# Performance work log

Measured on AMD Instinct MI355X. Metric: run time of the kernel, lower is better.

The kernel has to match this reference:

```python
import jax, jax.numpy as jnp
import numpy as np

L, CIN, CKV, E, H, D, NQ, NK = 3, 128, 256, 128, 8, 16, 4096, 1024
CLAMP_MAX = 65503.0  # torch.clamp(max=65503)
SCALE = 1.0 / (D * D)  # non-standard: 1 / projection_dim**2


def group_norm(x, w, b, groups, eps=1e-5):
    # x: [..., C, N]; w, b broadcastable to x.shape[:-1] (i.e. lead + (C,))
    lead = x.shape[:-2]
    C, N = x.shape[-2:]
    xg = x.reshape(lead + (groups, C // groups, N))
    mu = xg.mean(axis=(-2, -1), keepdims=True)
    var = ((xg - mu) ** 2).mean(axis=(-2, -1), keepdims=True)
    xn = ((xg - mu) * jax.lax.rsqrt(var + eps)).reshape(lead + (C, N))
    return xn * w[..., None] + b[..., None]


def split_heads(t):
    # [L, 1, E, N] -> [L, 1, H, N, D]
    l, b, e, n = t.shape
    return t.transpose(0, 1, 3, 2).reshape(l, b, n, H, D).transpose(0, 1, 3, 2, 4)


def setup_inputs():
    key = jax.random.key(0)
    ks = jax.random.split(key, 18)
    r = lambda k, s: jax.random.normal(k, s, dtype=jnp.float32)
    return {
        'x': r(ks[0], (1, CIN, NQ)),
        'x_global': r(ks[1], (L, CKV, NK)),
        'xyz': r(ks[2], (1, NQ, 3)),
        'xyz_global': r(ks[3], (L, NK, 3)),
        'gn1_w': r(ks[4], (CIN,)), 'gn1_b': r(ks[5], (CIN,)),
        'gn2_w': r(ks[6], (L, CKV)), 'gn2_b': r(ks[7], (L, CKV)),
        'qw': r(ks[8], (L, E, CIN)) * 0.05, 'qb': r(ks[9], (L, E)),
        'kw': r(ks[10], (L, E, CKV)) * 0.05, 'kb': r(ks[11], (L, E)),
        'vw': r(ks[12], (L, E, CKV)) * 0.05, 'vb': r(ks[13], (L, E)),
        'qgn_w': r(ks[14], (L, E)), 'qgn_b': r(ks[15], (L, E)),
        'cw': r(ks[16], (L, CIN, E)) * 0.05, 'cb': r(ks[17], (L, CIN)),
    }


def reference(x, x_global, xyz, xyz_global, gn1_w, gn1_b, gn2_w, gn2_b,
              qw, qb, kw, kb, vw, vb, qgn_w, qgn_b, cw, cb):
    # pre-norm of query features (shared across layers): [1, CIN, NQ]
    xq = jax.nn.relu(group_norm(x, gn1_w, gn1_b, 8))
    # per-source KV features: [L, 1, CKV, NK]
    xg = jax.nn.relu(group_norm(x_global[:, None], gn2_w[:, None], gn2_b[:, None], 16))

    # conv1d (kernel=1) projections + the shared q_gn GroupNorm(8, E)
    q = jnp.einsum('lec,bcn->lben', qw, xq) + qb[:, None, :, None]        # [L,1,E,NQ]
    q = group_norm(q, qgn_w[:, None], qgn_b[:, None], 8)
    k = jnp.einsum('lec,lbcn->lben', kw, xg) + kb[:, None, :, None]       # [L,1,E,NK]
    k = group_norm(k, qgn_w[:, None], qgn_b[:, None], 8)
    v = jnp.einsum('lec,lbcn->lben', vw, xg) + vb[:, None, :, None]       # [L,1,E,NK]
    v = group_norm(v, qgn_w[:, None], qgn_b[:, None], 8)

    qh, kh, vh = split_heads(q), split_heads(k), split_heads(v)           # [L,1,H,*,D]

    score = jnp.einsum('lbhqd,lbhkd->lbhqk', qh * SCALE, kh)              # [L,1,H,NQ,NK]
    score = jnp.minimum(score, CLAMP_MAX)
    w_att = jax.nn.softmax(score, axis=-1)
    o = jnp.einsum('lbhqk,lbhkd->lbhqd', w_att, vh)                        # [L,1,H,NQ,D]
    o = o.transpose(0, 1, 3, 2, 4).reshape(L, 1, NQ, E)                    # merge heads
    o = jnp.einsum('lbqe,loe->lbqo', o, cw) + cb[:, None, None, :]         # combine heads
    o = o.transpose(0, 1, 3, 2) + xq[None]                                 # [L,1,CIN,NQ], SA residual

    out = o.mean(axis=0) + x                                               # mean over sources + block residual
    return out, w_att[-1]                                                  # weight of last layer, as in torch loop
```

## Files before the change

kernel.cpp:

```cpp
#include <hip/hip_runtime.h>
#include <math.h>

constexpr int NQ = 4096, NK = 1024, CIN = 128, CKV = 256, E = 128, H = 8, D = 16, LAYERS = 3;
constexpr float SCALE = 1.0f / 256.0f;
constexpr float CLAMP_MAX = 65503.0f;
constexpr float LOG2E = 1.44269504088896340736f;
constexpr float CLAMP2 = CLAMP_MAX * LOG2E;

typedef __bf16 bf16x8 __attribute__((ext_vector_type(8)));
typedef __bf16 bf16x4 __attribute__((ext_vector_type(4)));
typedef float f32x16 __attribute__((ext_vector_type(16)));
typedef float f32x4 __attribute__((ext_vector_type(4)));

__device__ __forceinline__ float exp2_fast(float x) {
#if __has_builtin(__builtin_amdgcn_exp2f)
  return __builtin_amdgcn_exp2f(x);
#else
  return exp2f(x);
#endif
}

__device__ __forceinline__ void block_reduce2(float& a, float& b, float* red) {
#pragma unroll
  for (int off = 32; off > 0; off >>= 1) {
    a += __shfl_down(a, off, 64);
    b += __shfl_down(b, off, 64);
  }
  int lane = threadIdx.x & 63, wid = threadIdx.x >> 6;
  if (lane == 0) { red[wid * 2] = a; red[wid * 2 + 1] = b; }
  __syncthreads();
  if (threadIdx.x == 0) {
    float sa = 0.f, sb = 0.f;
#pragma unroll
    for (int w = 0; w < 4; w++) { sa += red[w * 2]; sb += red[w * 2 + 1]; }
    red[0] = sa; red[1] = sb;
  }
  __syncthreads();
  a = red[0]; b = red[1];
}

__global__ __launch_bounds__(256) void pre_partial(const float* __restrict__ x,
                                                   const float* __restrict__ xg,
                                                   float* __restrict__ acc) {
  __shared__ float red[8];
  int b = blockIdx.x, t = threadIdx.x;
  const float4* p;
  int aidx;
  if (b < 256) { p = (const float4*)x + (size_t)b * 512; aidx = b >> 5; }
  else { int i = b - 256; p = (const float4*)xg + (size_t)i * 512; aidx = 8 + (i >> 3); }
  float s = 0.f, sq = 0.f;
#pragma unroll
  for (int i = 0; i < 2; i++) {
    float4 v = p[t + i * 256];
    s += v.x + v.y + v.z + v.w;
    sq += v.x * v.x + v.y * v.y + v.z * v.z + v.w * v.w;
  }
  block_reduce2(s, sq, red);
  if (t == 0) {
    atomicAdd(&acc[aidx * 2], s);
    atomicAdd(&acc[aidx * 2 + 1], sq);
  }
}

__global__ __launch_bounds__(256) void stage_a(const float* __restrict__ x,
                                               const float* __restrict__ xg,
                                               const float* __restrict__ acc,
                                               const float* __restrict__ gn1w,
                                               const float* __restrict__ gn1b,
                                               const float* __restrict__ gn2w,
                                               const float* __restrict__ gn2b,
                                               const float* __restrict__ qw,
                                               const float* __restrict__ kw,
                                               const float* __restrict__ vw,
                                               __bf16* __restrict__ xq_t,
                                               __bf16* __restrict__ xg_t,
                                               __bf16* __restrict__ qwb,
                                               __bf16* __restrict__ kwb,
                                               __bf16* __restrict__ vwb) {
  int b = blockIdx.x, t = threadIdx.x;
  if (b >= 320) {
    int i = b - 320;
    const float* src; __bf16* dst; int off;
    if (i < 24)      { src = qw; dst = qwb; off = i * 2048; }
    else if (i < 72) { src = kw; dst = kwb; off = (i - 24) * 2048; }
    else             { src = vw; dst = vwb; off = (i - 72) * 2048; }
    int base = off + t * 8;
    float4 a = *(const float4*)(src + base);
    float4 c = *(const float4*)(src + base + 4);
    bf16x8 o = { (__bf16)a.x, (__bf16)a.y, (__bf16)a.z, (__bf16)a.w,
                 (__bf16)c.x, (__bf16)c.y, (__bf16)c.z, (__bf16)c.w };
    *(bf16x8*)(dst + base) = o;
    return;
  }
  __shared__ float T[128 * 36];
  const float* in; __bf16* out; int N, Cout, ccbase, n0, gbase;
  const float* gw; const float* gb; float inv;
  if (b < 128) {
    in = x; N = NQ; out = xq_t; Cout = 128; ccbase = 0; n0 = b * 32;
    gw = gn1w; gb = gn1b; gbase = 0; inv = 1.f / 65536.f;
  } else {
    int i = b - 128; int l = i / 64; int r = i % 64; int ch = r >> 5;
    n0 = (r & 31) * 32;
    in = xg + ((size_t)l * 256 + ch * 128) * 1024; N = NK;
    out = xg_t + (size_t)l * 1024 * 256; Cout = 256; ccbase = ch * 128;
    gw = gn2w + l * 256 + ch * 128; gb = gn2b + l * 256 + ch * 128;
    gbase = 8 + l * 16 + ch * 8; inv = 1.f / 16384.f;
  }
  int nq = t & 7, cbase = t >> 3;
#pragma unroll
  for (int i = 0; i < 4; i++) {
    int c = cbase + 32 * i;
    int g = gbase + (c >> 4);
    float mu = acc[2 * g] * inv;
    float rs = rsqrtf(acc[2 * g + 1] * inv - mu * mu + 1e-5f);
    float sc = gw[c] * rs, sh = gb[c] - mu * sc;
    float4 v = *(const float4*)(in + (size_t)c * N + n0 + nq * 4);
    float4 o;
    o.x = fmaxf(v.x * sc + sh, 0.f);
    o.y = fmaxf(v.y * sc + sh, 0.f);
    o.z = fmaxf(v.z * sc + sh, 0.f);
    o.w = fmaxf(v.w * sc + sh, 0.f);
    *(float4*)(T + c * 36 + nq * 4) = o;
  }
  __syncthreads();
  int n = t >> 3, c0 = (t & 7) * 16;
  bf16x8 o1, o2;
#pragma unroll
  for (int j = 0; j < 8; j++) {
    o1[j] = (__bf16)T[(c0 + j) * 36 + n];
    o2[j] = (__bf16)T[(c0 + 8 + j) * 36 + n];
  }
  __bf16* op = out + (size_t)(n0 + n) * Cout + ccbase + c0;
  *(bf16x8*)op = o1;
  *(bf16x8*)(op + 8) = o2;
}

template <int KSTEPS>
__device__ __forceinline__ void gemm_tile(const __bf16* __restrict__ A,
                                          const __bf16* __restrict__ Bm,
                                          int stride, f32x16& acc, int l31, int half) {
#pragma unroll
  for (int ks = 0; ks < KSTEPS; ks++) {
    bf16x8 af = *(const bf16x8*)(A + (size_t)l31 * stride + ks * 16 + half * 8);
    bf16x8 bf = *(const bf16x8*)(Bm + (size_t)l31 * stride + ks * 16 + half * 8);
    acc = __builtin_amdgcn_mfma_f32_32x32x16_bf16(af, bf, acc, 0, 0, 0);
  }
}

__global__ __launch_bounds__(256) void proj_mfma(const __bf16* __restrict__ xq_t,
                                                 const __bf16* __restrict__ xg_t,
                                                 const __bf16* __restrict__ qwb,
                                                 const __bf16* __restrict__ kwb,
                                                 const __bf16* __restrict__ vwb,
                                                 const float* __restrict__ qb,
                                                 const float* __restrict__ kb,
                                                 const float* __restrict__ vb,
                                                 __bf16* __restrict__ q_raw,
                                                 __bf16* __restrict__ k_raw,
                                                 __bf16* __restrict__ v_raw,
                                                 float* __restrict__ qgnAcc) {
  int t = threadIdx.x;
  int w = blockIdx.x * 4 + (t >> 6);
  int lane = t & 63, l31 = lane & 31, half = lane >> 5;
  f32x16 acc = {0.f,0.f,0.f,0.f,0.f,0.f,0.f,0.f,0.f,0.f,0.f,0.f,0.f,0.f,0.f,0.f};
  int mat, l, e0, n0, N;
  const __bf16* A; const __bf16* Bm; const float* bias;
  if (w < 1536) {
    mat = 0; l = w >> 9; int r = w & 511; e0 = (r & 3) * 32; n0 = (r >> 2) * 32;
    N = NQ; A = qwb + (size_t)l * 128 * 128; Bm = xq_t; bias = qb + l * 128;
  } else if (w < 1920) {
    mat = 1; int idx = w - 1536; l = idx >> 7; int r = idx & 127;
    e0 = (r & 3) * 32; n0 = (r >> 2) * 32;
    N = NK; A = kwb + (size_t)l * 128 * 256; Bm = xg_t + (size_t)l * 1024 * 256;
    bias = kb + l * 128;
  } else {
    mat = 2; int idx = w - 1920; l = idx >> 7; int r = idx & 127;
    e0 = (r & 3) * 32; n0 = (r >> 2) * 32;
    N = NK; A = vwb + (size_t)l * 128 * 256; Bm = xg_t + (size_t)l * 1024 * 256;
    bias = vb + l * 128;
  }
  if (mat == 0) {
    gemm_tile<8>(A + (size_t)e0 * 128, Bm + (size_t)n0 * 128, 128, acc, l31, half);
  } else {
    gemm_tile<16>(A + (size_t)e0 * 256, Bm + (size_t)n0 * 256, 256, acc, l31, half);
  }

  float vals[16];
  float s0 = 0.f, sq0 = 0.f, s1 = 0.f, sq1 = 0.f;
#pragma unroll
  for (int r = 0; r < 16; r++) {
    int row = (r & 3) + 8 * (r >> 2) + 4 * half;
    float v = acc[r] + bias[e0 + row];
    vals[r] = v;
    if (r < 8) { s0 += v; sq0 += v * v; } else { s1 += v; sq1 += v * v; }
  }
#pragma unroll
  for (int off = 1; off < 64; off <<= 1) {
    s0 += __shfl_xor(s0, off); sq0 += __shfl_xor(sq0, off);
    s1 += __shfl_xor(s1, off); sq1 += __shfl_xor(sq1, off);
  }
  int gbase = (mat == 0 ? 0 : (mat == 1 ? 24 : 48)) + l * 8 + (e0 >> 4);
  if (lane == 0) {
    atomicAdd(&qgnAcc[gbase * 2], s0);
    atomicAdd(&qgnAcc[gbase * 2 + 1], sq0);
    atomicAdd(&qgnAcc[(gbase + 1) * 2], s1);
    atomicAdd(&qgnAcc[(gbase + 1) * 2 + 1], sq1);
  }
  if (mat < 2) {
    __bf16* out = (mat == 0 ? q_raw : k_raw);
#pragma unroll
    for (int qd = 0; qd < 4; qd++) {
      int h = (e0 >> 4) + (qd >> 1);
      int d0 = 4 * half + 8 * (qd & 1);
      bf16x4 o;
#pragma unroll
      for (int j = 0; j < 4; j++) o[j] = (__bf16)vals[qd * 4 + j];
      *(bf16x4*)(out + ((size_t)(l * 8 + h) * N + n0 + l31) * 16 + d0) = o;
    }
  } else {
#pragma unroll
    for (int r = 0; r < 16; r++) {
      int row = (r & 3) + 8 * (r >> 2) + 4 * half;
      int h = (e0 >> 4) + (row >> 4);
      v_raw[((size_t)(l * 8 + h) * 16 + (row & 15)) * NK + n0 + l31] = (__bf16)vals[r];
    }
  }
}

__global__ __launch_bounds__(256) void qkv_affine(__bf16* __restrict__ q_raw,
                                                  __bf16* __restrict__ k_raw,
                                                  __bf16* __restrict__ v_raw,
                                                  const float* __restrict__ acc,
                                                  const float* __restrict__ gw,
                                                  const float* __restrict__ gb) {
  int b = blockIdx.x, t = threadIdx.x;
  if (b < 768) {
    int v8 = b * 256 + t;
    int d0 = (v8 & 1) * 8;
    int lh = (v8 >> 1) >> 12;
    int l = lh >> 3, h = lh & 7;
    int g = l * 8 + h;
    const float inv = 1.f / 65536.f;
    float mu = acc[2 * g] * inv;
    float rs = rsqrtf(acc[2 * g + 1] * inv - mu * mu + 1e-5f);
    const float EX = SCALE * LOG2E;
    bf16x8 vv = *(bf16x8*)(q_raw + (size_t)v8 * 8);
    bf16x8 o;
#pragma unroll
    for (int j = 0; j < 8; j++) {
      int cidx = l * 128 + h * 16 + d0 + j;
      float w0 = gw[cidx] * rs;
      o[j] = (__bf16)(((float)vv[j] * w0 + (gb[cidx] - mu * w0)) * EX);
    }
    *(bf16x8*)(q_raw + (size_t)v8 * 8) = o;
  } else if (b < 960) {
    int v8 = (b - 768) * 256 + t;
    int d0 = (v8 & 1) * 8;
    int lh = (v8 >> 1) >> 10;
    int l = lh >> 3, h = lh & 7;
    int g = 24 + l * 8 + h;
    const float inv = 1.f / 16384.f;
    float mu = acc[2 * g] * inv;
    float rs = rsqrtf(acc[2 * g + 1] * inv - mu * mu + 1e-5f);
    bf16x8 vv = *(bf16x8*)(k_raw + (size_t)v8 * 8);
    bf16x8 o;
#pragma unroll
    for (int j = 0; j < 8; j++) {
      int cidx = l * 128 + h * 16 + d0 + j;
      float w0 = gw[cidx] * rs;
      o[j] = (__bf16)((float)vv[j] * w0 + (gb[cidx] - mu * w0));
    }
    *(bf16x8*)(k_raw + (size_t)v8 * 8) = o;
  } else {
    int v8 = (b - 960) * 256 + t;
    int rest = v8 >> 7;
    int d = rest & 15, lh = rest >> 4;
    int l = lh >> 3, h = lh & 7;
    int g = 48 + l * 8 + h;
    const float inv = 1.f / 16384.f;
    float mu = acc[2 * g] * inv;
    float rs = rsqrtf(acc[2 * g + 1] * inv - mu * mu + 1e-5f);
    int cidx = l * 128 + h * 16 + d;
    float w0 = gw[cidx] * rs;
    float sh = gb[cidx] - mu * w0;
    bf16x8 vv = *(bf16x8*)(v_raw + (size_t)v8 * 8);
    bf16x8 o;
#pragma unroll
    for (int j = 0; j < 8; j++) o[j] = (__bf16)((float)vv[j] * w0 + sh);
    *(bf16x8*)(v_raw + (size_t)v8 * 8) = o;
  }
}

__global__ __launch_bounds__(256) void attn_kernel(const __bf16* __restrict__ qbf,
                                                   const __bf16* __restrict__ kbf,
                                                   const __bf16* __restrict__ vbf,
                                                   float* __restrict__ ob,
                                                   float* __restrict__ rinv_ws) {
  __shared__ __bf16 Pt[4][32 * 40];
  __shared__ float rinv_s[4][32];

  const int t = threadIdx.x;
  const int wv = t >> 6;
  const int lane = t & 63;
  const int l31 = lane & 31, half = lane >> 5, l15 = lane & 15, quad = lane >> 4;
  const int h = blockIdx.y, l = blockIdx.z;
  const int q0 = blockIdx.x * 128 + wv * 32;

  const __bf16* Qh = qbf + (size_t)(l * H + h) * NQ * D;
  const __bf16* Kh = kbf + (size_t)(l * H + h) * NK * D;
  const __bf16* Vh = vbf + (size_t)(l * H + h) * D * NK;

  const bf16x8 qfrag = *(const bf16x8*)(Qh + (size_t)(q0 + l31) * D + half * 8);

  f32x4 oa0 = {0.f, 0.f, 0.f, 0.f}, oa1 = {0.f, 0.f, 0.f, 0.f};
  float rsum[16];
#pragma unroll
  for (int r = 0; r < 16; ++r) rsum[r] = 0.f;

  __bf16* Pw = &Pt[wv][0];

  for (int c = 0; c < 32; ++c) {
    const int k0 = c * 32;
    bf16x8 kf = *(const bf16x8*)(Kh + (size_t)(k0 + l31) * D + half * 8);
    f32x16 s = {0.f,0.f,0.f,0.f,0.f,0.f,0.f,0.f,0.f,0.f,0.f,0.f,0.f,0.f,0.f,0.f};
    s = __builtin_amdgcn_mfma_f32_32x32x16_bf16(qfrag, kf, s, 0, 0, 0);
#pragma unroll
    for (int r = 0; r < 16; ++r) {
      float p = exp2_fast(fminf(s[r], CLAMP2));
      rsum[r] += p;
      int row = (r & 3) + 8 * (r >> 2) + 4 * half;
      Pw[row * 40 + l31] = (__bf16)p;
    }
    bf16x8 a0 = *(const bf16x8*)(Pw + l15 * 40 + quad * 8);
    bf16x8 a1 = *(const bf16x8*)(Pw + (16 + l15) * 40 + quad * 8);
    bf16x8 bv = *(const bf16x8*)(Vh + (size_t)l15 * NK + k0 + quad * 8);
    oa0 = __builtin_amdgcn_mfma_f32_16x16x32_bf16(a0, bv, oa0, 0, 0, 0);
    oa1 = __builtin_amdgcn_mfma_f32_16x16x32_bf16(a1, bv, oa1, 0, 0, 0);
  }

#pragma unroll
  for (int r = 0; r < 16; ++r) {
    float v = rsum[r];
    v += __shfl_xor(v, 1); v += __shfl_xor(v, 2); v += __shfl_xor(v, 4);
    v += __shfl_xor(v, 8); v += __shfl_xor(v, 16);
    rsum[r] = v;
  }
  if (l31 == 0) {
#pragma unroll
    for (int r = 0; r < 16; ++r)
      rinv_s[wv][(r & 3) + 8 * (r >> 2) + 4 * half] = 1.f / rsum[r];
  }

  float* Ow = (float*)Pw;
#pragma unroll
  for (int r = 0; r < 4; ++r) {
    int qa = quad * 4 + r;
    Ow[l15 * 36 + qa] = oa0[r] * rinv_s[wv][qa];
    Ow[l15 * 36 + 16 + qa] = oa1[r] * rinv_s[wv][16 + qa];
  }
  if (l == 2 && lane < 32)
    rinv_ws[(size_t)h * NQ + q0 + lane] = rinv_s[wv][lane];
  {
    int dd = lane >> 2, j = (lane & 3) * 8;
    float4 u0 = *(const float4*)(Ow + dd * 36 + j);
    float4 u1 = *(const float4*)(Ow + dd * 36 + j + 4);
    size_t rb = (size_t)(l * E + h * D + dd) * NQ + q0 + j;
    *(float4*)(ob + rb) = u0;
    *(float4*)(ob + rb + 4) = u1;
  }
}

__global__ __launch_bounds__(256) void wout_kernel(const __bf16* __restrict__ qbf,
                                                   const __bf16* __restrict__ kbf,
                                                   const float* __restrict__ rinv_ws,
                                                   float* __restrict__ wout) {
  const int t = threadIdx.x;
  const int wv = t >> 6;
  const int lane = t & 63;
  const int l31 = lane & 31, half = lane >> 5;
  const int h = blockIdx.y;
  const int q0 = blockIdx.x * 128 + wv * 32;
  const int kbase = blockIdx.z * 512;

  const __bf16* Qh = qbf + (size_t)(2 * H + h) * NQ * D;
  const __bf16* Kh = kbf + (size_t)(2 * H + h) * NK * D;
  const bf16x8 qfrag = *(const bf16x8*)(Qh + (size_t)(q0 + l31) * D + half * 8);

  float riv[16];
#pragma unroll
  for (int r = 0; r < 16; ++r)
    riv[r] = rinv_ws[(size_t)h * NQ + q0 + (r & 3) + 8 * (r >> 2) + 4 * half];

  for (int c = 0; c < 16; ++c) {
    const int k0 = kbase + c * 32;
    bf16x8 kf = *(const bf16x8*)(Kh + (size_t)(k0 + l31) * D + half * 8);
    f32x16 s = {0.f,0.f,0.f,0.f,0.f,0.f,0.f,0.f,0.f,0.f,0.f,0.f,0.f,0.f,0.f,0.f};
    s = __builtin_amdgcn_mfma_f32_32x32x16_bf16(qfrag, kf, s, 0, 0, 0);
#pragma unroll
    for (int r = 0; r < 16; ++r) {
      float p = exp2_fast(fminf(s[r], CLAMP2)) * riv[r];
      int row = (r & 3) + 8 * (r >> 2) + 4 * half;
      __builtin_nontemporal_store(p, &wout[(size_t)(h * NQ + q0 + row) * NK + k0 + l31]);
    }
  }
}

__global__ __launch_bounds__(256) void combine_kernel(const float* __restrict__ x,
                                                      const float* __restrict__ acc,
                                                      const float* __restrict__ gn1w,
                                                      const float* __restrict__ gn1b,
                                                      const float* __restrict__ ob,
                                                      const float* __restrict__ cw,
                                                      const float* __restrict__ cb,
                                                      float* __restrict__ out) {
  __shared__ float S[128 * 16];
  const int t = threadIdx.x;
  const int nt0 = blockIdx.x * 16;
  const int c0 = (t >> 2) * 2;
  const int nf = t & 3;
  float4 a0 = make_float4(0.f, 0.f, 0.f, 0.f);
  float4 a1 = make_float4(0.f, 0.f, 0.f, 0.f);
  for (int l = 0; l < LAYERS; l++) {
    if (l) __syncthreads();
#pragma unroll
    for (int i = 0; i < 2; i++) {
      int fid = i * 256 + t;
      int e = fid >> 2, pos = fid & 3;
      *(float4*)(S + e * 16 + pos * 4) =
          *(const float4*)(ob + ((size_t)l * E + e) * NQ + nt0 + pos * 4);
    }
    __syncthreads();
    const float* cwl = cw + (size_t)l * CIN * E;
#pragma unroll 8
    for (int e4 = 0; e4 < E / 4; e4++) {
      const int e = e4 * 4;
      float4 w0 = *(const float4*)(cwl + (size_t)c0 * E + e);
      float4 w1 = *(const float4*)(cwl + (size_t)(c0 + 1) * E + e);
      float4 s0 = *(const float4*)(S + (e + 0) * 16 + nf * 4);
      float4 s1 = *(const float4*)(S + (e + 1) * 16 + nf * 4);
      float4 s2 = *(const float4*)(S + (e + 2) * 16 + nf * 4);
      float4 s3 = *(const float4*)(S + (e + 3) * 16 + nf * 4);
      a0.x += w0.x * s0.x + w0.y * s1.x + w0.z * s2.x + w0.w * s3.x;
      a0.y += w0.x * s0.y + w0.y * s1.y + w0.z * s2.y + w0.w * s3.y;
      a0.z += w0.x * s0.z + w0.y * s1.z + w0.z * s2.z + w0.w * s3.z;
      a0.w += w0.x * s0.w + w0.y * s1.w + w0.z * s2.w + w0.w * s3.w;
      a1.x += w1.x * s0.x + w1.y * s1.x + w1.z * s2.x + w1.w * s3.x;
      a1.y += w1.x * s0.y + w1.y * s1.y + w1.z * s2.y + w1.w * s3.y;
      a1.z += w1.x * s0.z + w1.y * s1.z + w1.z * s2.z + w1.w * s3.z;
      a1.w += w1.x * s0.w + w1.y * s1.w + w1.z * s2.w + w1.w * s3.w;
    }
  }
  const float third = 1.f / 3.f;
#pragma unroll
  for (int i = 0; i < 2; i++) {
    int c = c0 + i;
    float4 a = i ? a1 : a0;
    float bsum = (cb[c] + cb[CIN + c] + cb[2 * CIN + c]) * third;
    int g = c >> 4;
    const float inv = 1.f / 65536.f;
    float mu = acc[2 * g] * inv;
    float rs = rsqrtf(acc[2 * g + 1] * inv - mu * mu + 1e-5f);
    float sc = gn1w[c] * rs, sh = gn1b[c] - mu * sc;
    size_t off = (size_t)c * NQ + nt0 + nf * 4;
    float4 xv = *(const float4*)(x + off);
    float4 o;
    o.x = xv.x + fmaxf(xv.x * sc + sh, 0.f) + a.x * third + bsum;
    o.y = xv.y + fmaxf(xv.y * sc + sh, 0.f) + a.y * third + bsum;
    o.z = xv.z + fmaxf(xv.z * sc + sh, 0.f) + a.z * third + bsum;
    o.w = xv.w + fmaxf(xv.w * sc + sh, 0.f) + a.w * third + bsum;
    *(float4*)(out + off) = o;
  }
}

extern "C" void kernel_launch(void* const* d_in, const int* in_sizes, int n_in,
                              void* d_out, int out_size, void* d_ws, size_t ws_size,
                              hipStream_t stream) {
  (void)in_sizes; (void)n_in; (void)out_size;
  const float* x    = (const float*)d_in[0];
  const float* xgi  = (const float*)d_in[1];
  const float* gn1w = (const float*)d_in[4];
  const float* gn1b = (const float*)d_in[5];
  const float* gn2w = (const float*)d_in[6];
  const float* gn2b = (const float*)d_in[7];
  const float* qw   = (const float*)d_in[8];
  const float* qb   = (const float*)d_in[9];
  const float* kw   = (const float*)d_in[10];
  const float* kb   = (const float*)d_in[11];
  const float* vw   = (const float*)d_in[12];
  const float* vb   = (const float*)d_in[13];
  const float* qgnw = (const float*)d_in[14];
  const float* qgnb = (const float*)d_in[15];
  const float* cw   = (const float*)d_in[16];
  const float* cb   = (const float*)d_in[17];

  float* ws = (float*)d_ws;
  __bf16* xq_t  = (__bf16*)ws;
  __bf16* xg_t  = (__bf16*)(ws + 262144);
  __bf16* qwb   = (__bf16*)(ws + 655360);
  __bf16* kwb   = (__bf16*)(ws + 679936);
  __bf16* vwb   = (__bf16*)(ws + 729088);
  __bf16* q_raw = (__bf16*)(ws + 778240);
  __bf16* k_raw = (__bf16*)(ws + 1564672);
  __bf16* v_raw = (__bf16*)(ws + 1761280);
  float*  ob    = ws + 1957888;
  float*  accAll = ws + 3530752;
  float*  rinv_ws = ws + 3531008;
  if (ws_size < (size_t)3563776 * sizeof(float)) return;

  float* qgnAcc = accAll + 112;
  float* outp = (float*)d_out;
  float* wout = outp + 524288;

  hipMemsetAsync(accAll, 0, 256 * sizeof(float), stream);

  pre_partial<<<640, 256, 0, stream>>>(x, xgi, accAll);

  stage_a<<<440, 256, 0, stream>>>(x, xgi, accAll, gn1w, gn1b, gn2w, gn2b,
                                   qw, kw, vw, xq_t, xg_t, qwb, kwb, vwb);

  proj_mfma<<<576, 256, 0, stream>>>(xq_t, xg_t, qwb, kwb, vwb, qb, kb, vb,
                                     q_raw, k_raw, v_raw, qgnAcc);

  qkv_affine<<<1152, 256, 0, stream>>>(q_raw, k_raw, v_raw, qgnAcc, qgnw, qgnb);

  attn_kernel<<<dim3(32, 8, 3), 256, 0, stream>>>(q_raw, k_raw, v_raw, ob, rinv_ws);

  combine_kernel<<<256, 256, 0, stream>>>(x, accAll, gn1w, gn1b, ob, cw, cb, outp);

  wout_kernel<<<dim3(32, 8, 2), 256, 0, stream>>>(q_raw, k_raw, rinv_ws, wout);
}
```

Measured before the change: 302.3 us.

## Fuse q/k/v group-norm affine into attention and merge combine with wout

Removes the separate qkv_affine pass and applies the q_gn normalization on the fly: Q once per fragment, K and V per chunk inside the attention and wout loops. It also merges combine_kernel and wout_kernel into one launch, split by block index. This removes a read-modify-write pass over q/k/v and two kernel launches. In exchange, K and V are renormalized redundantly by every query block, which adds per-iteration ALU work in the inner loop.

```diff
diff --git a/kernel.cpp b/kernel.cpp
--- a/kernel.cpp
+++ b/kernel.cpp
@@ -227,73 +227,12 @@
   }
 }
 
-__global__ __launch_bounds__(256) void qkv_affine(__bf16* __restrict__ q_raw,
-                                                  __bf16* __restrict__ k_raw,
-                                                  __bf16* __restrict__ v_raw,
-                                                  const float* __restrict__ acc,
-                                                  const float* __restrict__ gw,
-                                                  const float* __restrict__ gb) {
-  int b = blockIdx.x, t = threadIdx.x;
-  if (b < 768) {
-    int v8 = b * 256 + t;
-    int d0 = (v8 & 1) * 8;
-    int lh = (v8 >> 1) >> 12;
-    int l = lh >> 3, h = lh & 7;
-    int g = l * 8 + h;
-    const float inv = 1.f / 65536.f;
-    float mu = acc[2 * g] * inv;
-    float rs = rsqrtf(acc[2 * g + 1] * inv - mu * mu + 1e-5f);
-    const float EX = SCALE * LOG2E;
-    bf16x8 vv = *(bf16x8*)(q_raw + (size_t)v8 * 8);
-    bf16x8 o;
-#pragma unroll
-    for (int j = 0; j < 8; j++) {
-      int cidx = l * 128 + h * 16 + d0 + j;
-      float w0 = gw[cidx] * rs;
-      o[j] = (__bf16)(((float)vv[j] * w0 + (gb[cidx] - mu * w0)) * EX);
-    }
-    *(bf16x8*)(q_raw + (size_t)v8 * 8) = o;
-  } else if (b < 960) {
-    int v8 = (b - 768) * 256 + t;
-    int d0 = (v8 & 1) * 8;
-    int lh = (v8 >> 1) >> 10;
-    int l = lh >> 3, h = lh & 7;
-    int g = 24 + l * 8 + h;
-    const float inv = 1.f / 16384.f;
-    float mu = acc[2 * g] * inv;
-    float rs = rsqrtf(acc[2 * g + 1] * inv - mu * mu + 1e-5f);
-    bf16x8 vv = *(bf16x8*)(k_raw + (size_t)v8 * 8);
-    bf16x8 o;
-#pragma unroll
-    for (int j = 0; j < 8; j++) {
-      int cidx = l * 128 + h * 16 + d0 + j;
-      float w0 = gw[cidx] * rs;
-      o[j] = (__bf16)((float)vv[j] * w0 + (gb[cidx] - mu * w0));
-    }
-    *(bf16x8*)(k_raw + (size_t)v8 * 8) = o;
-  } else {
-    int v8 = (b - 960) * 256 + t;
-    int rest = v8 >> 7;
-    int d = rest & 15, lh = rest >> 4;
-    int l = lh >> 3, h = lh & 7;
-    int g = 48 + l * 8 + h;
-    const float inv = 1.f / 16384.f;
-    float mu = acc[2 * g] * inv;
-    float rs = rsqrtf(acc[2 * g + 1] * inv - mu * mu + 1e-5f);
-    int cidx = l * 128 + h * 16 + d;
-    float w0 = gw[cidx] * rs;
-    float sh = gb[cidx] - mu * w0;
-    bf16x8 vv = *(bf16x8*)(v_raw + (size_t)v8 * 8);
-    bf16x8 o;
-#pragma unroll
-    for (int j = 0; j < 8; j++) o[j] = (__bf16)((float)vv[j] * w0 + sh);
-    *(bf16x8*)(v_raw + (size_t)v8 * 8) = o;
-  }
-}
-
 __global__ __launch_bounds__(256) void attn_kernel(const __bf16* __restrict__ qbf,
                                                    const __bf16* __restrict__ kbf,
                                                    const __bf16* __restrict__ vbf,
+                                                   const float* __restrict__ qgnAcc,
+                                                   const float* __restrict__ qgnw,
+                                                   const float* __restrict__ qgnb,
                                                    float* __restrict__ ob,
                                                    float* __restrict__ rinv_ws) {
   __shared__ __bf16 Pt[4][32 * 40];
@@ -310,7 +249,32 @@
   const __bf16* Kh = kbf + (size_t)(l * H + h) * NK * D;
   const __bf16* Vh = vbf + (size_t)(l * H + h) * D * NK;
 
-  const bf16x8 qfrag = *(const bf16x8*)(Qh + (size_t)(q0 + l31) * D + half * 8);
+  const int gq = l * 8 + h, gk = 24 + l * 8 + h, gv = 48 + l * 8 + h;
+  const float invq = 1.f / 65536.f, invkv = 1.f / 16384.f;
+  const float muq = qgnAcc[2 * gq] * invq;
+  const float rsq = rsqrtf(qgnAcc[2 * gq + 1] * invq - muq * muq + 1e-5f);
+  const float muk = qgnAcc[2 * gk] * invkv;
+  const float rsk = rsqrtf(qgnAcc[2 * gk + 1] * invkv - muk * muk + 1e-5f);
+  const float muv = qgnAcc[2 * gv] * invkv;
+  const float rsv = rsqrtf(qgnAcc[2 * gv + 1] * invkv - muv * muv + 1e-5f);
+
+  const int cbase = l * 128 + h * 16;
+  float ka[8], kc[8];
+  bf16x8 qfrag;
+  {
+    const float EX = SCALE * LOG2E;
+    bf16x8 qraw = *(const bf16x8*)(Qh + (size_t)(q0 + l31) * D + half * 8);
+#pragma unroll
+    for (int j = 0; j < 8; j++) {
+      float w = qgnw[cbase + half * 8 + j], bb = qgnb[cbase + half * 8 + j];
+      float wq = w * rsq;
+      qfrag[j] = (__bf16)((float)qraw[j] * (wq * EX) + (bb - muq * wq) * EX);
+      float wk = w * rsk;
+      ka[j] = wk; kc[j] = bb - muk * wk;
+    }
+  }
+  const float va = qgnw[cbase + l15] * rsv;
+  const float vc = qgnb[cbase + l15] - muv * va;
 
   f32x4 oa0 = {0.f, 0.f, 0.f, 0.f}, oa1 = {0.f, 0.f, 0.f, 0.f};
   float rsum[16];
@@ -321,7 +285,10 @@
 
   for (int c = 0; c < 32; ++c) {
     const int k0 = c * 32;
-    bf16x8 kf = *(const bf16x8*)(Kh + (size_t)(k0 + l31) * D + half * 8);
+    bf16x8 kraw = *(const bf16x8*)(Kh + (size_t)(k0 + l31) * D + half * 8);
+    bf16x8 kf;
+#pragma unroll
+    for (int j = 0; j < 8; j++) kf[j] = (__bf16)((float)kraw[j] * ka[j] + kc[j]);
     f32x16 s = {0.f,0.f,0.f,0.f,0.f,0.f,0.f,0.f,0.f,0.f,0.f,0.f,0.f,0.f,0.f,0.f};
     s = __builtin_amdgcn_mfma_f32_32x32x16_bf16(qfrag, kf, s, 0, 0, 0);
 #pragma unroll
@@ -331,9 +298,12 @@
       int row = (r & 3) + 8 * (r >> 2) + 4 * half;
       Pw[row * 40 + l31] = (__bf16)p;
     }
+    bf16x8 vraw = *(const bf16x8*)(Vh + (size_t)l15 * NK + k0 + quad * 8);
+    bf16x8 bv;
+#pragma unroll
+    for (int j = 0; j < 8; j++) bv[j] = (__bf16)((float)vraw[j] * va + vc);
     bf16x8 a0 = *(const bf16x8*)(Pw + l15 * 40 + quad * 8);
     bf16x8 a1 = *(const bf16x8*)(Pw + (16 + l15) * 40 + quad * 8);
-    bf16x8 bv = *(const bf16x8*)(Vh + (size_t)l15 * NK + k0 + quad * 8);
     oa0 = __builtin_amdgcn_mfma_f32_16x16x32_bf16(a0, bv, oa0, 0, 0, 0);
     oa1 = __builtin_amdgcn_mfma_f32_16x16x32_bf16(a1, bv, oa1, 0, 0, 0);
   }
@@ -370,52 +340,80 @@
   }
 }
 
-__global__ __launch_bounds__(256) void wout_kernel(const __bf16* __restrict__ qbf,
+__global__ __launch_bounds__(256) void post_kernel(const __bf16* __restrict__ qbf,
                                                    const __bf16* __restrict__ kbf,
                                                    const float* __restrict__ rinv_ws,
+                                                   const float* __restrict__ qgnAcc,
+                                                   const float* __restrict__ qgnw,
+                                                   const float* __restrict__ qgnb,
+                                                   const float* __restrict__ x,
+                                                   const float* __restrict__ accAll,
+                                                   const float* __restrict__ gn1w,
+                                                   const float* __restrict__ gn1b,
+                                                   const float* __restrict__ ob,
+                                                   const float* __restrict__ cw,
+                                                   const float* __restrict__ cb,
+                                                   float* __restrict__ out,
                                                    float* __restrict__ wout) {
-  const int t = threadIdx.x;
-  const int wv = t >> 6;
-  const int lane = t & 63;
-  const int l31 = lane & 31, half = lane >> 5;
-  const int h = blockIdx.y;
-  const int q0 = blockIdx.x * 128 + wv * 32;
-  const int kbase = blockIdx.z * 512;
-
-  const __bf16* Qh = qbf + (size_t)(2 * H + h) * NQ * D;
-  const __bf16* Kh = kbf + (size_t)(2 * H + h) * NK * D;
-  const bf16x8 qfrag = *(const bf16x8*)(Qh + (size_t)(q0 + l31) * D + half * 8);
-
-  float riv[16];
-#pragma unroll
-  for (int r = 0; r < 16; ++r)
-    riv[r] = rinv_ws[(size_t)h * NQ + q0 + (r & 3) + 8 * (r >> 2) + 4 * half];
-
-  for (int c = 0; c < 16; ++c) {
-    const int k0 = kbase + c * 32;
-    bf16x8 kf = *(const bf16x8*)(Kh + (size_t)(k0 + l31) * D + half * 8);
-    f32x16 s = {0.f,0.f,0.f,0.f,0.f,0.f,0.f,0.f,0.f,0.f,0.f,0.f,0.f,0.f,0.f,0.f};
-    s = __builtin_amdgcn_mfma_f32_32x32x16_bf16(qfrag, kf, s, 0, 0, 0);
-#pragma unroll
-    for (int r = 0; r < 16; ++r) {
-      float p = exp2_fast(fminf(s[r], CLAMP2)) * riv[r];
-      int row = (r & 3) + 8 * (r >> 2) + 4 * half;
-      __builtin_nontemporal_store(p, &wout[(size_t)(h * NQ + q0 + row) * NK + k0 + l31]);
-    }
-  }
-}
-
-__global__ __launch_bounds__(256) void combine_kernel(const float* __restrict__ x,
-                                                      const float* __restrict__ acc,
-                                                      const float* __restrict__ gn1w,
-                                                      const float* __restrict__ gn1b,
-                                                      const float* __restrict__ ob,
-                                                      const float* __restrict__ cw,
-                                                      const float* __restrict__ cb,
-                                                      float* __restrict__ out) {
   __shared__ float S[128 * 16];
-  const int t = threadIdx.x;
-  const int nt0 = blockIdx.x * 16;
+  const int blk = blockIdx.x, t = threadIdx.x;
+  if (blk < 512) {
+    const int wv = t >> 6, lane = t & 63;
+    const int l31 = lane & 31, half = lane >> 5;
+    const int qtile = blk & 31, h = (blk >> 5) & 7, khalf = blk >> 8;
+    const int q0 = qtile * 128 + wv * 32;
+    const int kbase = khalf * 512;
+
+    const __bf16* Qh = qbf + (size_t)(2 * H + h) * NQ * D;
+    const __bf16* Kh = kbf + (size_t)(2 * H + h) * NK * D;
+
+    const int gq = 16 + h, gk = 24 + 16 + h;
+    const float invq = 1.f / 65536.f, invkv = 1.f / 16384.f;
+    const float muq = qgnAcc[2 * gq] * invq;
+    const float rsq = rsqrtf(qgnAcc[2 * gq + 1] * invq - muq * muq + 1e-5f);
+    const float muk = qgnAcc[2 * gk] * invkv;
+    const float rsk = rsqrtf(qgnAcc[2 * gk + 1] * invkv - muk * muk + 1e-5f);
+
+    const int cbase = 2 * 128 + h * 16;
+    float ka[8], kc[8];
+    bf16x8 qfrag;
+    {
+      const float EX = SCALE * LOG2E;
+      bf16x8 qraw = *(const bf16x8*)(Qh + (size_t)(q0 + l31) * D + half * 8);
+#pragma unroll
+      for (int j = 0; j < 8; j++) {
+        float w = qgnw[cbase + half * 8 + j], bb = qgnb[cbase + half * 8 + j];
+        float wq = w * rsq;
+        qfrag[j] = (__bf16)((float)qraw[j] * (wq * EX) + (bb - muq * wq) * EX);
+        float wk = w * rsk;
+        ka[j] = wk; kc[j] = bb - muk * wk;
+      }
+    }
+
+    float riv[16];
+#pragma unroll
+    for (int r = 0; r < 16; ++r)
+      riv[r] = rinv_ws[(size_t)h * NQ + q0 + (r & 3) + 8 * (r >> 2) + 4 * half];
+
+    for (int c = 0; c < 16; ++c) {
+      const int k0 = kbase + c * 32;
+      bf16x8 kraw = *(const bf16x8*)(Kh + (size_t)(k0 + l31) * D + half * 8);
+      bf16x8 kf;
+#pragma unroll
+      for (int j = 0; j < 8; j++) kf[j] = (__bf16)((float)kraw[j] * ka[j] + kc[j]);
+      f32x16 s = {0.f,0.f,0.f,0.f,0.f,0.f,0.f,0.f,0.f,0.f,0.f,0.f,0.f,0.f,0.f,0.f};
+      s = __builtin_amdgcn_mfma_f32_32x32x16_bf16(qfrag, kf, s, 0, 0, 0);
+#pragma unroll
+      for (int r = 0; r < 16; ++r) {
+        float p = exp2_fast(fminf(s[r], CLAMP2)) * riv[r];
+        int row = (r & 3) + 8 * (r >> 2) + 4 * half;
+        __builtin_nontemporal_store(p, &wout[(size_t)(h * NQ + q0 + row) * NK + k0 + l31]);
+      }
+    }
+    return;
+  }
+
+  const int nt0 = (blk - 512) * 16;
   const int c0 = (t >> 2) * 2;
   const int nf = t & 3;
   float4 a0 = make_float4(0.f, 0.f, 0.f, 0.f);
@@ -458,8 +456,8 @@
     float bsum = (cb[c] + cb[CIN + c] + cb[2 * CIN + c]) * third;
     int g = c >> 4;
     const float inv = 1.f / 65536.f;
-    float mu = acc[2 * g] * inv;
-    float rs = rsqrtf(acc[2 * g + 1] * inv - mu * mu + 1e-5f);
+    float mu = accAll[2 * g] * inv;
+    float rs = rsqrtf(accAll[2 * g + 1] * inv - mu * mu + 1e-5f);
     float sc = gn1w[c] * rs, sh = gn1b[c] - mu * sc;
     size_t off = (size_t)c * NQ + nt0 + nf * 4;
     float4 xv = *(const float4*)(x + off);
@@ -521,11 +519,9 @@
   proj_mfma<<<576, 256, 0, stream>>>(xq_t, xg_t, qwb, kwb, vwb, qb, kb, vb,
                                      q_raw, k_raw, v_raw, qgnAcc);
 
-  qkv_affine<<<1152, 256, 0, stream>>>(q_raw, k_raw, v_raw, qgnAcc, qgnw, qgnb);
-
-  attn_kernel<<<dim3(32, 8, 3), 256, 0, stream>>>(q_raw, k_raw, v_raw, ob, rinv_ws);
-
-  combine_kernel<<<256, 256, 0, stream>>>(x, accAll, gn1w, gn1b, ob, cw, cb, outp);
-
-  wout_kernel<<<dim3(32, 8, 2), 256, 0, stream>>>(q_raw, k_raw, rinv_ws, wout);
-}
+  attn_kernel<<<dim3(32, 8, 3), 256, 0, stream>>>(q_raw, k_raw, v_raw,
+                                                  qgnAcc, qgnw, qgnb, ob, rinv_ws);
+
+  post_kernel<<<768, 256, 0, stream>>>(q_raw, k_raw, rinv_ws, qgnAcc, qgnw, qgnb,
+                                       x, accAll, gn1w, gn1b, ob, cw, cb, outp, wout);
+}
```

Result: faster. 289.3 us (-4.3%).
